# Optimization experiments

Measured on AMD Instinct MI355X. Metric: run time of the kernel, lower is better.

The kernel has to match this reference:

```python
import jax, jax.numpy as jnp
import numpy as np

N_LAYERS = 3
FEATS = 128
POS = 3
M_DIM = 64
E_IN = 1 + 2 * FEATS          # 257 (rel_dist + x_i + x_j)
N_NODES = 20000
N_EDGES = 320000
LN_EPS = 1e-5


def _xavier(key, shape):
    fan_in, fan_out = shape[0], shape[1]
    std = (2.0 / (fan_in + fan_out)) ** 0.5
    return jax.random.normal(key, shape, dtype=jnp.float32) * std


def setup_inputs() -> dict:
    key = jax.random.key(0)
    ks = jax.random.split(key, 10)
    x = jax.random.normal(ks[0], (N_NODES, POS + FEATS), dtype=jnp.float32)
    edge_index = jax.random.randint(ks[1], (2, N_EDGES), 0, N_NODES)
    L = N_LAYERS
    def stack(k, shape):
        return jax.vmap(lambda kk: _xavier(kk, shape))(jax.random.split(k, L))
    params = {
        "ew1": stack(ks[2], (E_IN, 2 * E_IN)),      # edge_mlp linear 1
        "eb1": jnp.zeros((L, 2 * E_IN), jnp.float32),
        "ew2": stack(ks[3], (2 * E_IN, M_DIM)),      # edge_mlp linear 2
        "eb2": jnp.zeros((L, M_DIM), jnp.float32),
        "ng": jnp.ones((L, FEATS), jnp.float32),     # node LayerNorm gamma
        "nb": jnp.zeros((L, FEATS), jnp.float32),    # node LayerNorm beta
        "nw1": stack(ks[4], (FEATS + M_DIM, 2 * FEATS)),
        "nb1": jnp.zeros((L, 2 * FEATS), jnp.float32),
        "nw2": stack(ks[5], (2 * FEATS, FEATS)),
        "nb2": jnp.zeros((L, FEATS), jnp.float32),
        "cw1": stack(ks[6], (M_DIM, 4 * M_DIM)),
        "cb1": jnp.zeros((L, 4 * M_DIM), jnp.float32),
        "cw2": stack(ks[7], (4 * M_DIM, 1)),
        "cb2": jnp.zeros((L, 1), jnp.float32),
    }
    return {"x": x, "edge_index": edge_index, **params}


def _layer(x, edge_index, ew1, eb1, ew2, eb2, ng, nb, nw1, nb1, nw2, nb2,
           cw1, cb1, cw2, cb2):
    coors, feats = x[:, :POS], x[:, POS:]
    src, dst = edge_index[0], edge_index[1]
    # relative geometry per edge
    rel_coors = coors[src] - coors[dst]                       # [E, 3]
    rel_dist = jnp.sum(rel_coors * rel_coors, axis=-1, keepdims=True)  # [E, 1]
    # message MLP: cat[x_i (target), x_j (source), rel_dist]
    e_in = jnp.concatenate([feats[dst], feats[src], rel_dist], axis=-1)
    h = jax.nn.silu(e_in @ ew1 + eb1)
    m_ij = jax.nn.silu(h @ ew2 + eb2)                         # [E, m_dim]
    # coordinate update
    coor_w = jax.nn.silu(m_ij @ cw1 + cb1) @ cw2 + cb2        # [E, 1]
    mhat = jax.ops.segment_sum(coor_w * rel_coors, dst, num_segments=N_NODES)
    coors_out = coors + mhat
    # feature update (LayerNorm then MLP, residual)
    m_i = jax.ops.segment_sum(m_ij, dst, num_segments=N_NODES)
    mu = jnp.mean(feats, axis=-1, keepdims=True)
    var = jnp.mean((feats - mu) ** 2, axis=-1, keepdims=True)
    feats_n = (feats - mu) * jax.lax.rsqrt(var + LN_EPS) * ng + nb
    n_in = jnp.concatenate([feats_n, m_i], axis=-1)
    nh = jax.nn.silu(n_in @ nw1 + nb1) @ nw2 + nb2
    feats_out = feats + nh
    return jnp.concatenate([coors_out, feats_out], axis=-1)


def reference(x, edge_index, ew1, eb1, ew2, eb2, ng, nb, nw1, nb1, nw2, nb2,
              cw1, cb1, cw2, cb2):
    for l in range(N_LAYERS):
        x = _layer(x, edge_index,
                   ew1[l], eb1[l], ew2[l], eb2[l],
                   ng[l], nb[l], nw1[l], nb1[l], nw2[l], nb2[l],
                   cw1[l], cb1[l], cw2[l], cb2[l])
    return x
```

## Files before the change

kernel.cpp:

```cpp
#include <hip/hip_runtime.h>

typedef unsigned short u16;
typedef unsigned int   u32;
typedef __attribute__((ext_vector_type(2))) u32  u32x2;
typedef __attribute__((ext_vector_type(4))) u32  u32x4;
typedef __attribute__((ext_vector_type(8))) __bf16 bf16x8;
typedef __attribute__((ext_vector_type(4))) float  f32x4;

#define NN 20000
#define NE 320000
#define XD 131
#define F  128
#define MD 64
#define H1 514
#define H1P 544
#define NCH 17

#define GAS __attribute__((address_space(1)))
#define LAS __attribute__((address_space(3)))
#define LGKM0 asm volatile("s_waitcnt lgkmcnt(0)" ::: "memory")
#define VM0   asm volatile("s_waitcnt vmcnt(0)" ::: "memory")

__device__ __forceinline__ float silu(float a) {
    float e = __expf(-a);
    return a * __builtin_amdgcn_rcpf(1.0f + e);
}

__device__ __forceinline__ u16 f2bf(float f) {
    u32 u = __builtin_bit_cast(u32, f);
    return (u16)((u + 0x7FFFu + ((u >> 16) & 1u)) >> 16);
}
__device__ __forceinline__ u16 bfc(float f) { return __builtin_bit_cast(u16, (__bf16)f); }
__device__ __forceinline__ u32 pk2(float a, float b) {
    return (u32)bfc(a) | ((u32)bfc(b) << 16);
}
__device__ __forceinline__ bf16x8 mk8(u32 a, u32 b, u32 c, u32 d) {
    u32x4 t = {a, b, c, d};
    return __builtin_bit_cast(bf16x8, t);
}
__device__ __forceinline__ f32x4 mfma16(bf16x8 a, bf16x8 b, f32x4 c) {
    return __builtin_amdgcn_mfma_f32_16x16x32_bf16(a, b, c, 0, 0, 0);
}


__global__ void prep_w1(const float* __restrict__ ew1, const float* __restrict__ eb1,
                        u16* __restrict__ w1b, float* __restrict__ bias2) {
    int i = blockIdx.x * 256 + threadIdx.x;
    if (i >= 3 * H1P * 256) return;
    int k = i & 255;
    int n = (i >> 8) % H1P;
    int l = (i >> 8) / H1P;
    float v = (n < H1) ? ew1[(size_t)l * 257 * H1 + (size_t)k * H1 + n] : 0.f;
    w1b[(size_t)(l * H1P + n) * 256 + (k ^ ((n & 7) << 3))] = f2bf(v);
    if (k == 0) {
        bias2[(l * H1P + n) * 2 + 0] = (n < H1) ? eb1[l * H1 + n] : 0.f;
        bias2[(l * H1P + n) * 2 + 1] = (n < H1) ? ew1[(size_t)l * 257 * H1 + (size_t)256 * H1 + n] : 0.f;
    }
}

__global__ void prep_w2(const float* __restrict__ ew2, u16* __restrict__ w2b) {
    int i = blockIdx.x * 256 + threadIdx.x;
    if (i >= 3 * 64 * H1P) return;
    int k = i % H1P;
    int n = (i / H1P) & 63;
    int l = i / (H1P * 64);
    float v = (k < H1) ? ew2[(size_t)l * H1 * 64 + (size_t)k * 64 + n] : 0.f;
    w2b[(size_t)(l * 64 + n) * H1P + k] = f2bf(v);
}

__global__ void prep_cw1(const float* __restrict__ cw1, u16* __restrict__ cw1b) {
    int i = blockIdx.x * 256 + threadIdx.x;
    if (i >= 3 * 256 * 64) return;
    int k = i & 63;
    int n = (i >> 6) & 255;
    int l = i >> 14;
    cw1b[(size_t)l * 16384 + n * 64 + k] = f2bf(cw1[(size_t)l * 16384 + k * 256 + n]);
}

__global__ void prep_nw1(const float* __restrict__ nw1, u16* __restrict__ nw1b) {
    int i = blockIdx.x * 256 + threadIdx.x;
    if (i >= 3 * 256 * 192) return;
    int k = i % 192;
    int n = (i / 192) & 255;
    int l = i / (192 * 256);
    nw1b[(size_t)(l * 256 + n) * 192 + k] = f2bf(nw1[(size_t)l * 192 * 256 + (size_t)k * 256 + n]);
}

__global__ void prep_nw2(const float* __restrict__ nw2, u16* __restrict__ nw2b) {
    int i = blockIdx.x * 256 + threadIdx.x;
    if (i >= 3 * 128 * 256) return;
    int k = i & 255;
    int n = (i >> 8) & 127;
    int l = i >> 15;
    nw2b[(size_t)(l * 128 + n) * 256 + k] = f2bf(nw2[(size_t)l * 256 * 128 + (size_t)k * 128 + n]);
}

__global__ void x2bf(const float* __restrict__ xc, u32* __restrict__ xbf) {
    int i = blockIdx.x * 256 + threadIdx.x;
    if (i >= NN * 64) return;
    const int node = i >> 6, p = i & 63;
    const float a = xc[(size_t)node * XD + 3 + 2 * p];
    const float b = xc[(size_t)node * XD + 4 + 2 * p];
    xbf[(size_t)node * 64 + p] = pk2(a, b);
}


__global__ __launch_bounds__(256, 3) void edge_mfma(
    const float* __restrict__ x, const u16* __restrict__ xbf, const int* __restrict__ eidx,
    const char* __restrict__ w1b, const float* __restrict__ bias2,
    const char* __restrict__ w2b, const float* __restrict__ eb2,
    const char* __restrict__ cw1b, const float* __restrict__ cb1,
    const float* __restrict__ cw2, const float* __restrict__ cb2,
    float* __restrict__ m_i, float* __restrict__ mhat)
{
    __shared__ __align__(16) char LDS[45568];
    const int tid = threadIdx.x;
    const int w = tid >> 6, l = tid & 63, lg = l >> 4, lc = l & 15;
    const int ebase = blockIdx.x * 128 + w * 32;
    char*  HT  = LDS + 32768 + w * 2560;
    char*  MJ  = LDS + w * 4352;
    float* RDS = (float*)(LDS + 43008);
    int*   SDS = (int*)(LDS + 45056);
    char*  STG = LDS + w * 8192;

    if (l < 32) {
        const int e = ebase + l;
        const int s = eidx[e], d = eidx[NE + e];
        const float ax = x[(size_t)s * XD + 0] - x[(size_t)d * XD + 0];
        const float ay = x[(size_t)s * XD + 1] - x[(size_t)d * XD + 1];
        const float az = x[(size_t)s * XD + 2] - x[(size_t)d * XD + 2];
        f32x4 v = {ax, ay, az, ax * ax + ay * ay + az * az};
        *(f32x4*)(RDS + (w * 32 + l) * 4) = v;
        SDS[w * 32 + l] = d;
    }

    bf16x8 A[2][8];
    const int r4 = l >> 4;
    #pragma unroll
    for (int p = 0; p < 2; ++p) {
        const int ebs = (p ? 0 : NE) + ebase;
        #pragma unroll
        for (int j = 0; j < 8; ++j) {
            const int r = j * 4 + r4;
            const int node = eidx[ebs + r];
            const int cp = lc ^ (r & 7);
            __builtin_amdgcn_global_load_lds((const GAS u32*)(xbf + (size_t)node * 128 + cp * 8),
                                             (LAS u32*)(STG + j * 1024), 16, 0, 0);
        }
        VM0;
        #pragma unroll
        for (int kt = 0; kt < 4; ++kt)
            #pragma unroll
            for (int et = 0; et < 2; ++et) {
                const int R = et * 16 + lc;
                A[et][p * 4 + kt] = *(bf16x8*)(STG + R * 256 + ((kt * 64 + lg * 16) ^ ((R & 7) << 4)));
            }
        LGKM0;
    }

    float rd_e[2];
    rd_e[0] = RDS[(w * 32 + lc) * 4 + 3];
    rd_e[1] = RDS[(w * 32 + 16 + lc) * 4 + 3];
    LGKM0;

    __syncthreads();

    f32x4 c2[2][4];
    #pragma unroll
    for (int nt = 0; nt < 4; ++nt) {
        const float b = eb2[nt * 16 + lc];
        c2[0][nt] = (f32x4){b, b, b, b};
        c2[1][nt] = (f32x4){b, b, b, b};
    }

    {
        const char* g = w1b + (size_t)w * 4096;
        #pragma unroll
        for (int r = 0; r < 4; ++r)
            __builtin_amdgcn_global_load_lds((const GAS u32*)(g + r * 1024 + l * 16),
                                             (LAS u32*)(LDS + w * 4096 + r * 1024), 16, 0, 0);
    }

    const float* pB = bias2;
    #pragma unroll 1
    for (int ch = 0; ch < NCH; ++ch) {
        VM0;
        __syncthreads();
        if (ch + 1 < NCH) {
            const char* g = w1b + (size_t)(ch + 1) * 16384 + w * 4096;
            char* dst = LDS + ((ch + 1) & 1) * 16384 + w * 4096;
            #pragma unroll
            for (int r = 0; r < 4; ++r)
                __builtin_amdgcn_global_load_lds((const GAS u32*)(g + r * 1024 + l * 16),
                                                 (LAS u32*)(dst + r * 1024), 16, 0, 0);
        }
        char* Bc = LDS + (ch & 1) * 16384;

        #pragma unroll
        for (int nt = 0; nt < 2; ++nt) {
            const float* bp = pB + (nt * 16 + lg * 4) * 2;
            f32x4 q0 = *(const f32x4*)(bp);
            f32x4 q1 = *(const f32x4*)(bp + 4);
            f32x4 c10, c11;
            c10[0] = fmaf(rd_e[0], q0[1], q0[0]); c10[1] = fmaf(rd_e[0], q0[3], q0[2]);
            c10[2] = fmaf(rd_e[0], q1[1], q1[0]); c10[3] = fmaf(rd_e[0], q1[3], q1[2]);
            c11[0] = fmaf(rd_e[1], q0[1], q0[0]); c11[1] = fmaf(rd_e[1], q0[3], q0[2]);
            c11[2] = fmaf(rd_e[1], q1[1], q1[0]); c11[3] = fmaf(rd_e[1], q1[3], q1[2]);
            const int nl = nt * 16 + lc;
            #pragma unroll
            for (int kt = 0; kt < 8; ++kt) {
                bf16x8 Wf = *(bf16x8*)(Bc + nl * 512 + ((kt * 64 + lg * 16) ^ ((nl & 7) << 4)));
                c10 = mfma16(Wf, A[0][kt], c10);
                c11 = mfma16(Wf, A[1][kt], c11);
            }
            u32x2 v0, v1;
            v0[0] = pk2(silu(c10[0]), silu(c10[1])); v0[1] = pk2(silu(c10[2]), silu(c10[3]));
            v1[0] = pk2(silu(c11[0]), silu(c11[1])); v1[1] = pk2(silu(c11[2]), silu(c11[3]));
            *(u32x2*)(HT + lc * 80 + nt * 32 + lg * 8) = v0;
            *(u32x2*)(HT + (16 + lc) * 80 + nt * 32 + lg * 8) = v1;
        }
        LGKM0;
        bf16x8 A2[2];
        A2[0] = *(bf16x8*)(HT + lc * 80 + lg * 16);
        A2[1] = *(bf16x8*)(HT + (16 + lc) * 80 + lg * 16);
        #pragma unroll
        for (int nt = 0; nt < 4; ++nt) {
            bf16x8 Bw = __builtin_bit_cast(bf16x8,
                *(const u32x4*)(w2b + (size_t)(nt * 16 + lc) * 1088 + ch * 64 + lg * 16));
            c2[0][nt] = mfma16(A2[0], Bw, c2[0][nt]);
            c2[1][nt] = mfma16(A2[1], Bw, c2[1][nt]);
        }
        pB += 64;
    }

    __syncthreads();

    int dstn[2][4];
    #pragma unroll
    for (int mt = 0; mt < 2; ++mt)
        #pragma unroll
        for (int r = 0; r < 4; ++r)
            dstn[mt][r] = SDS[w * 32 + mt * 16 + lg * 4 + r];

    #pragma unroll
    for (int mt = 0; mt < 2; ++mt)
        #pragma unroll
        for (int nt = 0; nt < 4; ++nt)
            #pragma unroll
            for (int r = 0; r < 4; ++r) {
                const float v = silu(c2[mt][nt][r]);
                const int rowl = mt * 16 + lg * 4 + r;
                const int col  = nt * 16 + lc;
                *(u16*)(MJ + rowl * 136 + col * 2) = bfc(v);
                atomicAdd(m_i + (size_t)dstn[mt][r] * 64 + col, v);
            }
    LGKM0;

    bf16x8 A3[2][2];
    #pragma unroll
    for (int mt = 0; mt < 2; ++mt)
        #pragma unroll
        for (int kt = 0; kt < 2; ++kt)
            A3[mt][kt] = *(bf16x8*)(MJ + (mt * 16 + lc) * 136 + kt * 64 + lg * 16);

    float pw[2][4] = {{0.f, 0.f, 0.f, 0.f}, {0.f, 0.f, 0.f, 0.f}};
    #pragma unroll 4
    for (int ct3 = 0; ct3 < 16; ++ct3) {
        const int col = ct3 * 16 + lc;
        const float b = cb1[col];
        f32x4 c30 = {b, b, b, b}, c31 = {b, b, b, b};
        #pragma unroll
        for (int kt = 0; kt < 2; ++kt) {
            bf16x8 B = __builtin_bit_cast(bf16x8,
                *(const u32x4*)(cw1b + (size_t)col * 128 + kt * 64 + lg * 16));
            c30 = mfma16(A3[0][kt], B, c30);
            c31 = mfma16(A3[1][kt], B, c31);
        }
        const float w2v = cw2[col];
        #pragma unroll
        for (int r = 0; r < 4; ++r) {
            pw[0][r] = fmaf(silu(c30[r]), w2v, pw[0][r]);
            pw[1][r] = fmaf(silu(c31[r]), w2v, pw[1][r]);
        }
    }
    #pragma unroll
    for (int m = 1; m < 16; m <<= 1)
        #pragma unroll
        for (int mt = 0; mt < 2; ++mt)
            #pragma unroll
            for (int r = 0; r < 4; ++r)
                pw[mt][r] += __shfl_xor(pw[mt][r], m, 64);

    const float cb2v = cb2[0];
    if (lc < 3) {
        #pragma unroll
        for (int mt = 0; mt < 2; ++mt)
            #pragma unroll
            for (int r = 0; r < 4; ++r) {
                const int rowl = mt * 16 + lg * 4 + r;
                const float cwv = pw[mt][r] + cb2v;
                atomicAdd(mhat + (size_t)dstn[mt][r] * 3 + lc,
                          cwv * RDS[(w * 32 + rowl) * 4 + lc]);
            }
    }
}


__global__ __launch_bounds__(256, 2) void node_mfma(
    const float* __restrict__ xc, const float* __restrict__ m_i, const float* __restrict__ mh,
    const float* __restrict__ ng, const float* __restrict__ nb,
    const char* __restrict__ nw1b, const float* __restrict__ nb1,
    const char* __restrict__ nw2b, const float* __restrict__ nb2,
    float* __restrict__ xn)
{
    __shared__ __align__(16) char LDS[4 * 4352];
    const int tid = threadIdx.x;
    const int w = tid >> 6, l = tid & 63, lg = l >> 4, lc = l & 15;
    char* HB = LDS + w * 4352;
    const int nb0 = blockIdx.x * 128 + w * 32;

    int nodes[2]; bool valid[2];
    #pragma unroll
    for (int et = 0; et < 2; ++et) {
        int n = nb0 + et * 16 + lc;
        valid[et] = (n < NN);
        nodes[et] = valid[et] ? n : (NN - 1);
    }

    bf16x8 BF[2][6];
    #pragma unroll
    for (int et = 0; et < 2; ++et) {
        const float* xr = xc + (size_t)nodes[et] * XD + 3;
        float v[4][8];
        float s = 0.f, q = 0.f;
        #pragma unroll
        for (int kt = 0; kt < 4; ++kt) {
            const int k0 = kt * 32 + lg * 8;
            #pragma unroll
            for (int j = 0; j < 8; ++j) {
                const float t = xr[k0 + j];
                v[kt][j] = t; s += t; q = fmaf(t, t, q);
            }
        }
        s += __shfl_xor(s, 16, 64); s += __shfl_xor(s, 32, 64);
        q += __shfl_xor(q, 16, 64); q += __shfl_xor(q, 32, 64);
        const float mu = s * (1.f / 128.f);
        const float rs = rsqrtf(q * (1.f / 128.f) - mu * mu + 1e-5f);
        #pragma unroll
        for (int kt = 0; kt < 4; ++kt) {
            const int k0 = kt * 32 + lg * 8;
            float4 g0 = *(const float4*)(ng + k0), g1 = *(const float4*)(ng + k0 + 4);
            float4 b0 = *(const float4*)(nb + k0), b1 = *(const float4*)(nb + k0 + 4);
            const u32 u0 = pk2((v[kt][0] - mu) * rs * g0.x + b0.x, (v[kt][1] - mu) * rs * g0.y + b0.y);
            const u32 u1 = pk2((v[kt][2] - mu) * rs * g0.z + b0.z, (v[kt][3] - mu) * rs * g0.w + b0.w);
            const u32 u2 = pk2((v[kt][4] - mu) * rs * g1.x + b1.x, (v[kt][5] - mu) * rs * g1.y + b1.y);
            const u32 u3 = pk2((v[kt][6] - mu) * rs * g1.z + b1.z, (v[kt][7] - mu) * rs * g1.w + b1.w);
            BF[et][kt] = mk8(u0, u1, u2, u3);
        }
        const float* mr = m_i + (size_t)nodes[et] * 64;
        #pragma unroll
        for (int kt2 = 0; kt2 < 2; ++kt2) {
            float4 a = *(const float4*)(mr + kt2 * 32 + lg * 8);
            float4 b = *(const float4*)(mr + kt2 * 32 + lg * 8 + 4);
            BF[et][4 + kt2] = mk8(pk2(a.x, a.y), pk2(a.z, a.w), pk2(b.x, b.y), pk2(b.z, b.w));
        }
    }

    f32x4 a2[8][2];
    #pragma unroll
    for (int ct2 = 0; ct2 < 8; ++ct2) {
        f32x4 b = *(const f32x4*)(nb2 + ct2 * 16 + lg * 4);
        a2[ct2][0] = b; a2[ct2][1] = b;
    }

    #pragma unroll 1
    for (int g = 0; g < 4; ++g) {
        f32x4 a1[4][2];
        #pragma unroll
        for (int ct = 0; ct < 4; ++ct) {
            f32x4 b = *(const f32x4*)(nb1 + g * 64 + ct * 16 + lg * 4);
            a1[ct][0] = b; a1[ct][1] = b;
        }
        #pragma unroll
        for (int ct = 0; ct < 4; ++ct)
            #pragma unroll
            for (int kt = 0; kt < 6; ++kt) {
                bf16x8 Aw = __builtin_bit_cast(bf16x8, *(const u32x4*)(
                    nw1b + (size_t)(g * 64 + ct * 16 + lc) * 384 + kt * 64 + lg * 16));
                a1[ct][0] = mfma16(Aw, BF[0][kt], a1[ct][0]);
                a1[ct][1] = mfma16(Aw, BF[1][kt], a1[ct][1]);
            }
        #pragma unroll
        for (int ct = 0; ct < 4; ++ct)
            #pragma unroll
            for (int et = 0; et < 2; ++et) {
                f32x4 c = a1[ct][et];
                u32 v0 = pk2(silu(c[0]), silu(c[1]));
                u32 v1 = pk2(silu(c[2]), silu(c[3]));
                *(u32*)(HB + (et * 16 + lc) * 136 + ct * 32 + lg * 8) = v0;
                *(u32*)(HB + (et * 16 + lc) * 136 + ct * 32 + lg * 8 + 4) = v1;
            }
        LGKM0;
        __builtin_amdgcn_sched_barrier(0);
        bf16x8 B2[2][2];
        #pragma unroll
        for (int et = 0; et < 2; ++et)
            #pragma unroll
            for (int kt2 = 0; kt2 < 2; ++kt2) {
                u32 a = *(u32*)(HB + (et * 16 + lc) * 136 + kt2 * 64 + lg * 16);
                u32 b = *(u32*)(HB + (et * 16 + lc) * 136 + kt2 * 64 + lg * 16 + 4);
                u32 c = *(u32*)(HB + (et * 16 + lc) * 136 + kt2 * 64 + lg * 16 + 8);
                u32 d = *(u32*)(HB + (et * 16 + lc) * 136 + kt2 * 64 + lg * 16 + 12);
                B2[et][kt2] = mk8(a, b, c, d);
            }
        #pragma unroll
        for (int ct2 = 0; ct2 < 8; ++ct2)
            #pragma unroll
            for (int kt2 = 0; kt2 < 2; ++kt2) {
                bf16x8 Aw = __builtin_bit_cast(bf16x8, *(const u32x4*)(
                    nw2b + (size_t)(ct2 * 16 + lc) * 512 + (g * 64 + kt2 * 32 + lg * 8) * 2));
                a2[ct2][0] = mfma16(Aw, B2[0][kt2], a2[ct2][0]);
                a2[ct2][1] = mfma16(Aw, B2[1][kt2], a2[ct2][1]);
            }
        LGKM0;
        __builtin_amdgcn_sched_barrier(0);
    }

    #pragma unroll
    for (int et = 0; et < 2; ++et) {
        if (!valid[et]) continue;
        const size_t nr = (size_t)nodes[et] * XD;
        #pragma unroll
        for (int ct2 = 0; ct2 < 8; ++ct2)
            #pragma unroll
            for (int r = 0; r < 4; ++r) {
                const int col = ct2 * 16 + lg * 4 + r;
                xn[nr + 3 + col] = a2[ct2][et][r] + xc[nr + 3 + col];
            }
    }
    for (int idx = tid; idx < 384; idx += 256) {
        const int n = blockIdx.x * 128 + idx / 3;
        const int d = idx - (idx / 3) * 3;
        if (n < NN)
            xn[(size_t)n * XD + d] = xc[(size_t)n * XD + d] + mh[n * 3 + d];
    }
}


extern "C" void kernel_launch(void* const* d_in, const int* in_sizes, int n_in,
                              void* d_out, int out_size, void* d_ws, size_t ws_size,
                              hipStream_t stream) {
    const float* x_in = (const float*)d_in[0];
    const int*   eidx = (const int*)  d_in[1];
    const float* ew1  = (const float*)d_in[2];
    const float* eb1  = (const float*)d_in[3];
    const float* ew2  = (const float*)d_in[4];
    const float* eb2  = (const float*)d_in[5];
    const float* ng   = (const float*)d_in[6];
    const float* nb   = (const float*)d_in[7];
    const float* nw1  = (const float*)d_in[8];
    const float* nb1  = (const float*)d_in[9];
    const float* nw2  = (const float*)d_in[10];
    const float* nb2  = (const float*)d_in[11];
    const float* cw1  = (const float*)d_in[12];
    const float* cb1  = (const float*)d_in[13];
    const float* cw2  = (const float*)d_in[14];
    const float* cb2  = (const float*)d_in[15];
    float* out = (float*)d_out;

    char* ws = (char*)d_ws;
    size_t off = 0;
    auto alloc = [&](size_t bytes) { char* p = ws + off; off = (off + bytes + 255) & ~255ull; return p; };
    float* mi    = (float*)alloc((size_t)NN * MD * 4);
    float* mh    = (float*)alloc((size_t)NN * 3 * 4);
    u32*   xbf   = (u32*)  alloc((size_t)NN * 256);
    float* bias2 = (float*)alloc((size_t)3 * H1P * 8);
    char*  w1b   = alloc((size_t)3 * H1P * 512);
    char*  w2b   = alloc((size_t)3 * 64 * 1088);
    char*  cw1b  = alloc((size_t)3 * 256 * 128);
    char*  nw1b  = alloc((size_t)3 * 256 * 384);
    char*  nw2b  = alloc((size_t)3 * 128 * 512);

    prep_w1 <<<(3 * H1P * 256 + 255) / 256, 256, 0, stream>>>(ew1, eb1, (u16*)w1b, bias2);
    prep_w2 <<<(3 * 64 * H1P + 255) / 256, 256, 0, stream>>>(ew2, (u16*)w2b);
    prep_cw1<<<(3 * 256 * 64 + 255) / 256, 256, 0, stream>>>(cw1, (u16*)cw1b);
    prep_nw1<<<(3 * 256 * 192 + 255) / 256, 256, 0, stream>>>(nw1, (u16*)nw1b);
    prep_nw2<<<(3 * 128 * 256 + 255) / 256, 256, 0, stream>>>(nw2, (u16*)nw2b);

    for (int l = 0; l < 3; ++l) {
        const float* xc = (l == 0) ? x_in : out;
        float*       xn = out;
        hipMemsetAsync(mi, 0, (size_t)NN * MD * 4, stream);
        hipMemsetAsync(mh, 0, (size_t)NN * 3 * 4, stream);
        x2bf<<<(NN * 64 + 255) / 256, 256, 0, stream>>>(xc, xbf);
        edge_mfma<<<NE / 128, 256, 0, stream>>>(
            xc, (const u16*)xbf, eidx,
            w1b + (size_t)l * H1P * 512, bias2 + (size_t)l * H1P * 2,
            w2b + (size_t)l * 64 * 1088, eb2 + (size_t)l * 64,
            cw1b + (size_t)l * 256 * 128, cb1 + (size_t)l * 256,
            cw2 + (size_t)l * 256, cb2 + l,
            mi, mh);
        node_mfma<<<(NN + 127) / 128, 256, 0, stream>>>(
            xc, mi, mh,
            ng + (size_t)l * F, nb + (size_t)l * F,
            nw1b + (size_t)l * 256 * 384, nb1 + (size_t)l * 256,
            nw2b + (size_t)l * 128 * 512, nb2 + (size_t)l * F,
            xn);
    }
}
```

Measured before the change: 804.8 us.

## Replace m_i atomic scatter with CSR gather reduction over bf16 edge messages

Builds a CSR index of edges grouped by destination node once per call (histogram, scan, fill). The edge kernel then writes per-edge m_ij rows as bf16 to global memory instead of issuing float atomicAdds into m_i, and a new reduce_mi kernel sums each node's incoming rows. The goal is to remove the heavy atomic contention, 64 atomics per edge, and the per-layer memset of m_i. In exchange it adds an extra kernel launch per layer, a single-block scan, and about 40MB of extra global traffic per layer. Summation now happens on bf16-rounded messages, and the atomics path remains as a fallback when the workspace is too small.

Measured after the change: 925.6 us. 1.15x slower.

```diff
diff --git a/kernel.cpp b/kernel.cpp
--- a/kernel.cpp
+++ b/kernel.cpp
@@ -105,13 +105,76 @@
 }
 
 
+__global__ void csr_hist(const int* __restrict__ eidx, int* __restrict__ cnt) {
+    int e = blockIdx.x * 256 + threadIdx.x;
+    if (e < NE) atomicAdd(&cnt[eidx[NE + e]], 1);
+}
+
+__global__ void csr_scan(const int* __restrict__ cnt, int* __restrict__ rowp) {
+    __shared__ int ps[1024];
+    const int t = threadIdx.x;
+    const int base = t * 20;
+    int loc[20];
+    int s = 0;
+    #pragma unroll
+    for (int i = 0; i < 20; ++i) {
+        const int idx = base + i;
+        const int c = (idx < NN) ? cnt[idx] : 0;
+        loc[i] = s;
+        s += c;
+    }
+    ps[t] = s;
+    __syncthreads();
+    for (int off = 1; off < 1024; off <<= 1) {
+        int v = (t >= off) ? ps[t - off] : 0;
+        __syncthreads();
+        ps[t] += v;
+        __syncthreads();
+    }
+    const int segbase = (t > 0) ? ps[t - 1] : 0;
+    #pragma unroll
+    for (int i = 0; i < 20; ++i) {
+        const int idx = base + i;
+        if (idx < NN) rowp[idx] = segbase + loc[i];
+    }
+    if (t == 1023) rowp[NN] = ps[1023];
+}
+
+__global__ void csr_fill(const int* __restrict__ eidx, const int* __restrict__ rowp,
+                         int* __restrict__ fill, int* __restrict__ eids) {
+    int e = blockIdx.x * 256 + threadIdx.x;
+    if (e >= NE) return;
+    const int d = eidx[NE + e];
+    const int pos = atomicAdd(&fill[d], 1);
+    eids[rowp[d] + pos] = e;
+}
+
+
+__global__ __launch_bounds__(256, 4) void reduce_mi(
+    const u16* __restrict__ gmij, const int* __restrict__ rowp,
+    const int* __restrict__ eids, float* __restrict__ m_i) {
+    const int tid = threadIdx.x;
+    const int n = blockIdx.x * 4 + (tid >> 6);
+    const int c = tid & 63;
+    if (n >= NN) return;
+    const int b = rowp[n], e = rowp[n + 1];
+    float acc = 0.f;
+    for (int j = b; j < e; ++j) {
+        const int eid = eids[j];
+        const u16 v = gmij[(size_t)eid * 64 + c];
+        acc += __builtin_bit_cast(float, (u32)v << 16);
+    }
+    m_i[(size_t)n * 64 + c] = acc;
+}
+
+
 __global__ __launch_bounds__(256, 3) void edge_mfma(
     const float* __restrict__ x, const u16* __restrict__ xbf, const int* __restrict__ eidx,
     const char* __restrict__ w1b, const float* __restrict__ bias2,
     const char* __restrict__ w2b, const float* __restrict__ eb2,
     const char* __restrict__ cw1b, const float* __restrict__ cb1,
     const float* __restrict__ cw2, const float* __restrict__ cb2,
-    float* __restrict__ m_i, float* __restrict__ mhat)
+    float* __restrict__ m_i, float* __restrict__ mhat, u16* __restrict__ gmij)
 {
     __shared__ __align__(16) char LDS[45568];
     const int tid = threadIdx.x;
@@ -252,9 +315,19 @@
                 const int rowl = mt * 16 + lg * 4 + r;
                 const int col  = nt * 16 + lc;
                 *(u16*)(MJ + rowl * 136 + col * 2) = bfc(v);
-                atomicAdd(m_i + (size_t)dstn[mt][r] * 64 + col, v);
+                if (!gmij) atomicAdd(m_i + (size_t)dstn[mt][r] * 64 + col, v);
             }
     LGKM0;
+
+    if (gmij) {
+        u16* grow = gmij + (size_t)ebase * 64;
+        #pragma unroll
+        for (int i = 0; i < 4; ++i) {
+            const int row = i * 8 + (l >> 3);
+            u32x4 v = *(u32x4*)(MJ + row * 136 + (l & 7) * 16);
+            *(u32x4*)(grow + (size_t)row * 64 + (l & 7) * 8) = v;
+        }
+    }
 
     bf16x8 A3[2][2];
     #pragma unroll
@@ -480,6 +553,12 @@
     char*  cw1b  = alloc((size_t)3 * 256 * 128);
     char*  nw1b  = alloc((size_t)3 * 256 * 384);
     char*  nw2b  = alloc((size_t)3 * 128 * 512);
+    u16* gmij = (u16*)alloc((size_t)NE * 64 * 2);
+    int* rowp = (int*) alloc((size_t)(NN + 1) * 4);
+    int* eids = (int*) alloc((size_t)NE * 4);
+    int* cnt  = (int*) alloc((size_t)NN * 4);
+    int* fillp= (int*) alloc((size_t)NN * 4);
+    const bool two = (off <= ws_size);
 
     prep_w1 <<<(3 * H1P * 256 + 255) / 256, 256, 0, stream>>>(ew1, eb1, (u16*)w1b, bias2);
     prep_w2 <<<(3 * 64 * H1P + 255) / 256, 256, 0, stream>>>(ew2, (u16*)w2b);
@@ -487,10 +566,18 @@
     prep_nw1<<<(3 * 256 * 192 + 255) / 256, 256, 0, stream>>>(nw1, (u16*)nw1b);
     prep_nw2<<<(3 * 128 * 256 + 255) / 256, 256, 0, stream>>>(nw2, (u16*)nw2b);
 
+    if (two) {
+        hipMemsetAsync(cnt,  0, (size_t)NN * 4, stream);
+        hipMemsetAsync(fillp,0, (size_t)NN * 4, stream);
+        csr_hist<<<(NE + 255) / 256, 256, 0, stream>>>(eidx, cnt);
+        csr_scan<<<1, 1024, 0, stream>>>(cnt, rowp);
+        csr_fill<<<(NE + 255) / 256, 256, 0, stream>>>(eidx, rowp, fillp, eids);
+    }
+
     for (int l = 0; l < 3; ++l) {
         const float* xc = (l == 0) ? x_in : out;
         float*       xn = out;
-        hipMemsetAsync(mi, 0, (size_t)NN * MD * 4, stream);
+        if (!two) hipMemsetAsync(mi, 0, (size_t)NN * MD * 4, stream);
         hipMemsetAsync(mh, 0, (size_t)NN * 3 * 4, stream);
         x2bf<<<(NN * 64 + 255) / 256, 256, 0, stream>>>(xc, xbf);
         edge_mfma<<<NE / 128, 256, 0, stream>>>(
@@ -499,7 +586,9 @@
             w2b + (size_t)l * 64 * 1088, eb2 + (size_t)l * 64,
             cw1b + (size_t)l * 256 * 128, cb1 + (size_t)l * 256,
             cw2 + (size_t)l * 256, cb2 + l,
-            mi, mh);
+            mi, mh, two ? gmij : (u16*)nullptr);
+        if (two)
+            reduce_mi<<<(NN + 3) / 4, 256, 0, stream>>>(gmij, rowp, eids, mi);
         node_mfma<<<(NN + 127) / 128, 256, 0, stream>>>(
             xc, mi, mh,
             ng + (size_t)l * F, nb + (size_t)l * F,
```
